# Kernel tuning notes

Hardware: AMD Instinct MI355X
Metric: run time of the kernel (lower is better)

Reference implementation:

```python
import jax, jax.numpy as jnp
import numpy as np

D_IN = 1024
D_OUT = 1024
SEQ = 4096


def setup_inputs() -> dict:
    key = jax.random.key(0)
    kx, kq, kk, kv = jax.random.split(key, 4)
    s = 1.0 / np.sqrt(D_IN)
    return {
        "x": jax.random.normal(kx, (SEQ, D_IN), dtype=jnp.float32),
        # nn.Linear weights: shape [d_out, d_in], applied as x @ W.T
        "W_q": jax.random.uniform(kq, (D_OUT, D_IN), dtype=jnp.float32, minval=-s, maxval=s),
        "W_k": jax.random.uniform(kk, (D_OUT, D_IN), dtype=jnp.float32, minval=-s, maxval=s),
        "W_v": jax.random.uniform(kv, (D_OUT, D_IN), dtype=jnp.float32, minval=-s, maxval=s),
    }


def reference(x, W_q, W_k, W_v):
    # QKV projections (no bias)
    q = x @ W_q.T  # [N, d_out]
    k = x @ W_k.T
    v = x @ W_v.T
    d_k = k.shape[-1]
    scores = (q @ k.T) / jnp.sqrt(jnp.asarray(d_k, x.dtype))  # [N, N]
    attn = jax.nn.softmax(scores, axis=1)
    n = attn.shape[0]
    mask = jnp.tril(jnp.ones((n, n), dtype=attn.dtype))
    causal = attn * mask
    causal = causal / jnp.sum(causal, axis=1, keepdims=True)
    return causal @ v  # [N, d_out]
```

## Files before the change

kernel.cpp:

```cpp
#include <hip/hip_runtime.h>
#include <hip/hip_bf16.h>
#include <stdint.h>
#include <math.h>

#define SEQ 4096
#define DIM 1024

typedef __attribute__((ext_vector_type(8))) __bf16 bf16x8;
typedef __attribute__((ext_vector_type(4))) float f32x4;
typedef __attribute__((ext_vector_type(8))) unsigned short u16x8;

__device__ __forceinline__ unsigned short f2bf(float f) {
  unsigned int u = __float_as_uint(f);
  u = (u + 0x7FFFu + ((u >> 16) & 1u)) >> 16;
  return (unsigned short)u;
}

__device__ __forceinline__ int swz(int o) { return o ^ (((o >> 7) & 7) << 4); }

template <int N> __device__ __forceinline__ void wait_vm() {
  if constexpr (N == 0) asm volatile("s_waitcnt vmcnt(0)" ::: "memory");
  else if constexpr (N == 2) asm volatile("s_waitcnt vmcnt(2)" ::: "memory");
  else if constexpr (N == 4) asm volatile("s_waitcnt vmcnt(4)" ::: "memory");
  else if constexpr (N == 6) asm volatile("s_waitcnt vmcnt(6)" ::: "memory");
  else if constexpr (N == 8) asm volatile("s_waitcnt vmcnt(8)" ::: "memory");
}

__global__ void __launch_bounds__(256) cvt_all(const float* __restrict__ x,
                                               const float* __restrict__ wq,
                                               const float* __restrict__ wk,
                                               const float* __restrict__ wv,
                                               unsigned short* __restrict__ xb,
                                               unsigned short* __restrict__ wqk,
                                               unsigned short* __restrict__ wvb) {
  const int bid = blockIdx.x;
  const float* src;
  unsigned short* dst;
  size_t base;
  if (bid < 2048)      { src = x;  dst = xb;                base = (size_t)bid * 2048; }
  else if (bid < 2560) { src = wq; dst = wqk;               base = (size_t)(bid - 2048) * 2048; }
  else if (bid < 3072) { src = wk; dst = wqk + 1024 * 1024; base = (size_t)(bid - 2560) * 2048; }
  else                 { src = wv; dst = wvb;               base = (size_t)(bid - 3072) * 2048; }
  size_t i = base + (size_t)threadIdx.x * 8;
  float4 a = *reinterpret_cast<const float4*>(src + i);
  float4 b = *reinterpret_cast<const float4*>(src + i + 4);
  u16x8 o;
  o[0] = f2bf(a.x); o[1] = f2bf(a.y); o[2] = f2bf(a.z); o[3] = f2bf(a.w);
  o[4] = f2bf(b.x); o[5] = f2bf(b.y); o[6] = f2bf(b.z); o[7] = f2bf(b.w);
  *reinterpret_cast<u16x8*>(dst + i) = o;
}

__global__ void __launch_bounds__(256) proj_qk(const unsigned short* __restrict__ A,
                                               const unsigned short* __restrict__ B,
                                               unsigned short* __restrict__ C) {
  constexpr int lda = DIM, ldb = DIM, ldc = 2048;
  const int tr = blockIdx.x >> 4, tc = blockIdx.x & 15;

  __shared__ __align__(16) unsigned short As[2][128 * 64];
  __shared__ __align__(16) unsigned short Bs[2][128 * 64];

  const int tid = threadIdx.x;
  const int lane = tid & 63;
  const int wid = tid >> 6;
  const int wr = wid >> 1, wc = wid & 1;
  const int l15 = lane & 15;
  const int kq = lane >> 4;

  f32x4 acc[4][4];
  #pragma unroll
  for (int m = 0; m < 4; ++m)
    #pragma unroll
    for (int n = 0; n < 4; ++n)
      acc[m][n] = (f32x4){0.f, 0.f, 0.f, 0.f};

  const unsigned short* Abase = A + (size_t)tr * 128 * lda;
  const unsigned short* Bbase = B + (size_t)tc * 128 * ldb;

  auto stage = [&](int buf, int kt) {
    const int k0 = kt << 6;
    #pragma unroll
    for (int i = 0; i < 4; ++i) {
      const int o = (i * 256 + tid) * 16;
      const int cs = (swz(o) >> 4) & 7;
      const unsigned short* ga = Abase + (size_t)(o >> 7) * lda + k0 + cs * 8;
      const unsigned short* gb = Bbase + (size_t)(o >> 7) * ldb + k0 + cs * 8;
      __builtin_amdgcn_global_load_lds(
          (const __attribute__((address_space(1))) unsigned int*)ga,
          (__attribute__((address_space(3))) unsigned int*)((char*)&As[buf][0] + o), 16, 0, 0);
      __builtin_amdgcn_global_load_lds(
          (const __attribute__((address_space(1))) unsigned int*)gb,
          (__attribute__((address_space(3))) unsigned int*)((char*)&Bs[buf][0] + o), 16, 0, 0);
    }
  };

  stage(0, 0);
  int cur = 0;
  for (int kt = 0; kt < 16; ++kt) {
    if (kt + 1 < 16) { stage(cur ^ 1, kt + 1); wait_vm<8>(); }
    else wait_vm<0>();
    __builtin_amdgcn_s_barrier();

    bf16x8 af[4][2], bv[4][2];
    #pragma unroll
    for (int m = 0; m < 4; ++m)
      #pragma unroll
      for (int ks = 0; ks < 2; ++ks) {
        const int row = wr * 64 + m * 16 + l15;
        af[m][ks] = *reinterpret_cast<const bf16x8*>(
            (const char*)&As[cur][0] + swz(row * 128 + kq * 16 + ks * 64));
      }
    #pragma unroll
    for (int n = 0; n < 4; ++n)
      #pragma unroll
      for (int ks = 0; ks < 2; ++ks) {
        const int row = wc * 64 + n * 16 + l15;
        bv[n][ks] = *reinterpret_cast<const bf16x8*>(
            (const char*)&Bs[cur][0] + swz(row * 128 + kq * 16 + ks * 64));
      }
    #pragma unroll
    for (int m = 0; m < 4; ++m)
      #pragma unroll
      for (int n = 0; n < 4; ++n) {
        acc[m][n] = __builtin_amdgcn_mfma_f32_16x16x32_bf16(af[m][0], bv[n][0], acc[m][n], 0, 0, 0);
        acc[m][n] = __builtin_amdgcn_mfma_f32_16x16x32_bf16(af[m][1], bv[n][1], acc[m][n], 0, 0, 0);
      }
    __builtin_amdgcn_s_barrier();
    cur ^= 1;
  }

  const int rbase = tr * 128 + wr * 64 + kq * 4;
  const int cbase = tc * 128 + wc * 64 + l15;
  #pragma unroll
  for (int m = 0; m < 4; ++m)
    #pragma unroll
    for (int n = 0; n < 4; ++n)
      #pragma unroll
      for (int i = 0; i < 4; ++i)
        C[(size_t)(rbase + m * 16 + i) * ldc + cbase + n * 16] = f2bf(acc[m][n][i]);
}

__global__ void __launch_bounds__(1024) qkt_vt(const unsigned short* __restrict__ Q,
                                               const unsigned short* __restrict__ K,
                                               unsigned short* __restrict__ S,
                                               const unsigned short* __restrict__ wvb,
                                               const unsigned short* __restrict__ xb,
                                               unsigned short* __restrict__ vt) {
  __shared__ __align__(16) unsigned short As[2][256 * 64];
  __shared__ __align__(16) unsigned short Bs[2][256 * 64];

  const int bid = ((blockIdx.x & 7) << 5) + (blockIdx.x >> 3);
  const int tid = threadIdx.x;
  const int lane = tid & 63;
  const int wid = tid >> 6;
  const int wr = wid >> 2;
  const int wc = wid & 3;
  const int l15 = lane & 15;
  const int kq = lane >> 4;

  if (bid < 136) {
    int tr = (int)((sqrtf(8.0f * bid + 1.0f) - 1.0f) * 0.5f);
    while ((tr + 1) * (tr + 2) / 2 <= bid) ++tr;
    while (tr * (tr + 1) / 2 > bid) --tr;
    const int tc = bid - tr * (tr + 1) / 2;

    constexpr int LDA = 2 * DIM, LDC = SEQ;
    constexpr float SCALE = 0.03125f;

    const unsigned short* Abase = Q + (size_t)tr * 256 * LDA;
    const unsigned short* Bbase = K + (size_t)tc * 256 * LDA;

    f32x4 acc[4][4];
    #pragma unroll
    for (int m = 0; m < 4; ++m)
      #pragma unroll
      for (int n = 0; n < 4; ++n)
        acc[m][n] = (f32x4){0.f, 0.f, 0.f, 0.f};

    auto stage4 = [&](int buf, int kt) {
      const int k0 = kt << 6;
      #pragma unroll
      for (int i = 0; i < 2; ++i) {
        const int ot = (i * 1024 + tid) << 4;
        const int row = ot >> 7;
        const int cs = (swz(ot) >> 4) & 7;
        const unsigned short* ga = Abase + (size_t)row * LDA + k0 + cs * 8;
        const unsigned short* gb = Bbase + (size_t)row * LDA + k0 + cs * 8;
        __builtin_amdgcn_global_load_lds(
            (const __attribute__((address_space(1))) unsigned int*)ga,
            (__attribute__((address_space(3))) unsigned int*)((char*)&As[buf][0] + ot), 16, 0, 0);
        __builtin_amdgcn_global_load_lds(
            (const __attribute__((address_space(1))) unsigned int*)gb,
            (__attribute__((address_space(3))) unsigned int*)((char*)&Bs[buf][0] + ot), 16, 0, 0);
      }
    };

    stage4(0, 0);
    int cur = 0;
    #pragma unroll 1
    for (int kt = 0; kt < 16; ++kt) {
      if (kt + 1 < 16) { stage4(cur ^ 1, kt + 1); wait_vm<4>(); }
      else wait_vm<0>();
      __builtin_amdgcn_s_barrier();

      #pragma unroll
      for (int ks = 0; ks < 2; ++ks) {
        bf16x8 a[4], b[4];
        #pragma unroll
        for (int m = 0; m < 4; ++m) {
          const int row = wr * 64 + m * 16 + l15;
          a[m] = *reinterpret_cast<const bf16x8*>(
              (const char*)&As[cur][0] + swz(row * 128 + kq * 16 + ks * 64));
        }
        #pragma unroll
        for (int n = 0; n < 4; ++n) {
          const int row = wc * 64 + n * 16 + l15;
          b[n] = *reinterpret_cast<const bf16x8*>(
              (const char*)&Bs[cur][0] + swz(row * 128 + kq * 16 + ks * 64));
        }
        __builtin_amdgcn_s_setprio(1);
        #pragma unroll
        for (int m = 0; m < 4; ++m)
          #pragma unroll
          for (int n = 0; n < 4; ++n)
            acc[m][n] = __builtin_amdgcn_mfma_f32_16x16x32_bf16(a[m], b[n], acc[m][n], 0, 0, 0);
        __builtin_amdgcn_s_setprio(0);
      }
      __builtin_amdgcn_s_barrier();
      cur ^= 1;
    }

    const int rb = tr * 256 + wr * 64 + kq * 4;
    const int cb = tc * 256 + wc * 64 + l15;
    #pragma unroll
    for (int m = 0; m < 4; ++m)
      #pragma unroll
      for (int n = 0; n < 4; ++n)
        #pragma unroll
        for (int i = 0; i < 4; ++i)
          S[(size_t)(rb + m * 16 + i) * LDC + cb + n * 16] = f2bf(acc[m][n][i] * SCALE);
    return;
  }

  unsigned short* A0 = &As[0][0];
  unsigned short* B0 = &Bs[0][0];

  for (int t = bid - 136; t < 256; t += 120) {
    const int tr = t >> 5, tc = t & 31;
    const unsigned short* Abase = wvb + (size_t)tr * 128 * DIM;
    const unsigned short* Bbase = xb + (size_t)tc * 128 * DIM;

    f32x4 acc[2][2];
    #pragma unroll
    for (int m = 0; m < 2; ++m)
      #pragma unroll
      for (int n = 0; n < 2; ++n)
        acc[m][n] = (f32x4){0.f, 0.f, 0.f, 0.f};

    auto stage = [&](int buf, int kt) {
      const int k0 = kt << 6;
      const int o = tid << 4;
      const int cs = (swz(o) >> 4) & 7;
      const unsigned short* ga = Abase + (size_t)(o >> 7) * DIM + k0 + cs * 8;
      const unsigned short* gb = Bbase + (size_t)(o >> 7) * DIM + k0 + cs * 8;
      __builtin_amdgcn_global_load_lds(
          (const __attribute__((address_space(1))) unsigned int*)ga,
          (__attribute__((address_space(3))) unsigned int*)((char*)(A0 + buf * 128 * 64) + o), 16, 0, 0);
      __builtin_amdgcn_global_load_lds(
          (const __attribute__((address_space(1))) unsigned int*)gb,
          (__attribute__((address_space(3))) unsigned int*)((char*)(B0 + buf * 128 * 64) + o), 16, 0, 0);
    };

    stage(0, 0);
    int cur = 0;
    for (int kt = 0; kt < 16; ++kt) {
      if (kt + 1 < 16) { stage(cur ^ 1, kt + 1); wait_vm<2>(); }
      else wait_vm<0>();
      __builtin_amdgcn_s_barrier();

      bf16x8 af[2][2], bv[2][2];
      #pragma unroll
      for (int m = 0; m < 2; ++m)
        #pragma unroll
        for (int ks = 0; ks < 2; ++ks) {
          const int row = wr * 32 + m * 16 + l15;
          af[m][ks] = *reinterpret_cast<const bf16x8*>(
              (const char*)(A0 + cur * 128 * 64) + swz(row * 128 + kq * 16 + ks * 64));
        }
      #pragma unroll
      for (int n = 0; n < 2; ++n)
        #pragma unroll
        for (int ks = 0; ks < 2; ++ks) {
          const int row = wc * 32 + n * 16 + l15;
          bv[n][ks] = *reinterpret_cast<const bf16x8*>(
              (const char*)(B0 + cur * 128 * 64) + swz(row * 128 + kq * 16 + ks * 64));
        }
      #pragma unroll
      for (int m = 0; m < 2; ++m)
        #pragma unroll
        for (int n = 0; n < 2; ++n) {
          acc[m][n] = __builtin_amdgcn_mfma_f32_16x16x32_bf16(af[m][0], bv[n][0], acc[m][n], 0, 0, 0);
          acc[m][n] = __builtin_amdgcn_mfma_f32_16x16x32_bf16(af[m][1], bv[n][1], acc[m][n], 0, 0, 0);
        }
      __builtin_amdgcn_s_barrier();
      cur ^= 1;
    }

    const int rbase = tr * 128 + wr * 32 + kq * 4;
    const int cbase = tc * 128 + wc * 32 + l15;
    #pragma unroll
    for (int m = 0; m < 2; ++m)
      #pragma unroll
      for (int n = 0; n < 2; ++n)
        #pragma unroll
        for (int i = 0; i < 4; ++i)
          vt[(size_t)(rbase + m * 16 + i) * SEQ + cbase + n * 16] = f2bf(acc[m][n][i]);
    __builtin_amdgcn_s_barrier();
  }
}

__global__ void __launch_bounds__(256) pv_kernel(const unsigned short* __restrict__ A,
                                                 const unsigned short* __restrict__ B,
                                                 float* __restrict__ C,
                                                 float* __restrict__ P1, float* __restrict__ P2,
                                                 float* __restrict__ P3) {
  constexpr int BM = 64;
  constexpr int lda = SEQ, ldb = SEQ, ldc = DIM;
  int tc = blockIdx.x, tr = blockIdx.y;
  const int s = blockIdx.z;
  const int ltiles = tr + 1;
  int kt0 = s * 16;
  if (kt0 >= ltiles) return;
  const int nt = min(ltiles, kt0 + 16) - kt0;

  __shared__ __align__(16) unsigned short As[2][BM * 64];
  __shared__ __align__(16) unsigned short Bs[2][128 * 64];

  const int tid = threadIdx.x;
  const int lane = tid & 63;
  const int wid = tid >> 6;
  const int wr = wid >> 1, wc = wid & 1;
  const int l15 = lane & 15;
  const int kq = lane >> 4;

  f32x4 acc[2][4];
  #pragma unroll
  for (int m = 0; m < 2; ++m)
    #pragma unroll
    for (int n = 0; n < 4; ++n)
      acc[m][n] = (f32x4){0.f, 0.f, 0.f, 0.f};

  const unsigned short* Abase = A + (size_t)tr * BM * lda;
  const unsigned short* Bbase = B + (size_t)tc * 128 * ldb;

  auto stage = [&](int buf, int ktabs) {
    const int k0 = ktabs << 6;
    #pragma unroll
    for (int i = 0; i < 2; ++i) {
      const int o = (i * 256 + tid) * 16;
      const int cs = (swz(o) >> 4) & 7;
      const unsigned short* g = Abase + (size_t)(o >> 7) * lda + k0 + cs * 8;
      __builtin_amdgcn_global_load_lds(
          (const __attribute__((address_space(1))) unsigned int*)g,
          (__attribute__((address_space(3))) unsigned int*)((char*)&As[buf][0] + o), 16, 0, 0);
    }
    #pragma unroll
    for (int i = 0; i < 4; ++i) {
      const int o = (i * 256 + tid) * 16;
      const int cs = (swz(o) >> 4) & 7;
      const unsigned short* g = Bbase + (size_t)(o >> 7) * ldb + k0 + cs * 8;
      __builtin_amdgcn_global_load_lds(
          (const __attribute__((address_space(1))) unsigned int*)g,
          (__attribute__((address_space(3))) unsigned int*)((char*)&Bs[buf][0] + o), 16, 0, 0);
    }
  };

  stage(0, kt0);
  int cur = 0;
  for (int kt = 0; kt < nt; ++kt) {
    if (kt + 1 < nt) { stage(cur ^ 1, kt0 + kt + 1); wait_vm<6>(); }
    else wait_vm<0>();
    __builtin_amdgcn_s_barrier();

    bf16x8 af[2][2], bv[4][2];
    #pragma unroll
    for (int m = 0; m < 2; ++m)
      #pragma unroll
      for (int ks = 0; ks < 2; ++ks) {
        const int row = wr * 32 + m * 16 + l15;
        af[m][ks] = *reinterpret_cast<const bf16x8*>(
            (const char*)&As[cur][0] + swz(row * 128 + kq * 16 + ks * 64));
      }
    #pragma unroll
    for (int n = 0; n < 4; ++n)
      #pragma unroll
      for (int ks = 0; ks < 2; ++ks) {
        const int row = wc * 64 + n * 16 + l15;
        bv[n][ks] = *reinterpret_cast<const bf16x8*>(
            (const char*)&Bs[cur][0] + swz(row * 128 + kq * 16 + ks * 64));
      }
    #pragma unroll
    for (int m = 0; m < 2; ++m)
      #pragma unroll
      for (int n = 0; n < 4; ++n) {
        acc[m][n] = __builtin_amdgcn_mfma_f32_16x16x32_bf16(af[m][0], bv[n][0], acc[m][n], 0, 0, 0);
        acc[m][n] = __builtin_amdgcn_mfma_f32_16x16x32_bf16(af[m][1], bv[n][1], acc[m][n], 0, 0, 0);
      }
    __builtin_amdgcn_s_barrier();
    cur ^= 1;
  }

  float* fdst = C;
  int rowoff = 0;
  if (s == 1) { fdst = P1; rowoff = 1024; }
  else if (s == 2) { fdst = P2; rowoff = 2048; }
  else if (s == 3) { fdst = P3; rowoff = 3072; }
  const int rbase = tr * BM + wr * 32 + kq * 4;
  const int cbase = tc * 128 + wc * 64 + l15;
  #pragma unroll
  for (int m = 0; m < 2; ++m)
    #pragma unroll
    for (int n = 0; n < 4; ++n)
      #pragma unroll
      for (int i = 0; i < 4; ++i)
        fdst[(size_t)(rbase + m * 16 + i - rowoff) * ldc + cbase + n * 16] = acc[m][n][i];
}

__global__ void __launch_bounds__(256) reduce_kernel(float* __restrict__ out,
                                                     const float* __restrict__ p1,
                                                     const float* __restrict__ p2,
                                                     const float* __restrict__ p3) {
  const int b = blockIdx.x;
  const size_t e = ((size_t)b * 1024) + threadIdx.x * 4;
  f32x4 acc = *reinterpret_cast<f32x4*>(out + (size_t)1024 * 1024 + e);
  acc += *reinterpret_cast<const f32x4*>(p1 + e);
  if (b >= 1024) acc += *reinterpret_cast<const f32x4*>(p2 + e - (size_t)1024 * 1024);
  if (b >= 2048) acc += *reinterpret_cast<const f32x4*>(p3 + e - (size_t)2048 * 1024);
  *reinterpret_cast<f32x4*>(out + (size_t)1024 * 1024 + e) = acc;
}

__global__ void __launch_bounds__(512) softmax_causal2(unsigned short* __restrict__ S) {
  const int g = threadIdx.x >> 8;
  const int row = g ? (SEQ - 1 - blockIdx.x) : blockIdx.x;
  const int tid = threadIdx.x & 255;
  const int lane = threadIdx.x & 63;
  const int wid = (threadIdx.x >> 6) & 3;
  const int limit = ((row >> 6) + 1) << 6;
  unsigned short* Srow = S + (size_t)row * SEQ;

  float vals[16];
  bool act[2];
  #pragma unroll
  for (int i = 0; i < 2; ++i) {
    const int j0 = (tid + i * 256) * 8;
    act[i] = j0 < limit;
    if (act[i]) {
      const uint4 w = *reinterpret_cast<const uint4*>(Srow + j0);
      const unsigned int wb[4] = {w.x, w.y, w.z, w.w};
      #pragma unroll
      for (int e = 0; e < 4; ++e) {
        vals[i * 8 + 2 * e]     = __uint_as_float(wb[e] << 16);
        vals[i * 8 + 2 * e + 1] = __uint_as_float(wb[e] & 0xFFFF0000u);
      }
    } else {
      #pragma unroll
      for (int e = 0; e < 8; ++e) vals[i * 8 + e] = -1e30f;
    }
  }

  float m = -1e30f;
  #pragma unroll
  for (int i = 0; i < 2; ++i)
    #pragma unroll
    for (int e = 0; e < 8; ++e) {
      int j = (tid + i * 256) * 8 + e;
      if (j <= row) m = fmaxf(m, vals[i * 8 + e]);
    }
  #pragma unroll
  for (int off = 32; off > 0; off >>= 1) m = fmaxf(m, __shfl_xor(m, off));
  __shared__ float redm[2][4], reds[2][4];
  if (lane == 0) redm[g][wid] = m;
  __syncthreads();
  m = fmaxf(fmaxf(redm[g][0], redm[g][1]), fmaxf(redm[g][2], redm[g][3]));

  float s = 0.f;
  float ev[16];
  #pragma unroll
  for (int i = 0; i < 2; ++i)
    #pragma unroll
    for (int e = 0; e < 8; ++e) {
      int j = (tid + i * 256) * 8 + e;
      float ex = (j <= row) ? __expf(vals[i * 8 + e] - m) : 0.f;
      ev[i * 8 + e] = ex;
      s += ex;
    }
  #pragma unroll
  for (int off = 32; off > 0; off >>= 1) s += __shfl_xor(s, off);
  if (lane == 0) reds[g][wid] = s;
  __syncthreads();
  s = reds[g][0] + reds[g][1] + reds[g][2] + reds[g][3];
  const float inv = 1.f / s;

  #pragma unroll
  for (int i = 0; i < 2; ++i) {
    if (!act[i]) continue;
    u16x8 o;
    #pragma unroll
    for (int e = 0; e < 8; ++e) o[e] = f2bf(ev[i * 8 + e] * inv);
    *reinterpret_cast<u16x8*>(Srow + (tid + i * 256) * 8) = o;
  }
}

extern "C" void kernel_launch(void* const* d_in, const int* in_sizes, int n_in,
                              void* d_out, int out_size, void* d_ws, size_t ws_size,
                              hipStream_t stream) {
  const float* x  = (const float*)d_in[0];
  const float* Wq = (const float*)d_in[1];
  const float* Wk = (const float*)d_in[2];
  const float* Wv = (const float*)d_in[3];
  float* out = (float*)d_out;

  char* ws = (char*)d_ws;
  const size_t MB = 1u << 20;
  unsigned short* xb   = (unsigned short*)(ws + 0 * MB);
  unsigned short* wqk  = (unsigned short*)(ws + 8 * MB);
  unsigned short* wvb  = (unsigned short*)(ws + 12 * MB);
  unsigned short* qkb  = (unsigned short*)(ws + 14 * MB);
  unsigned short* vt   = (unsigned short*)(ws + 30 * MB);
  unsigned short* S    = (unsigned short*)(ws + 38 * MB);
  float* p1 = (float*)(ws + 0 * MB);
  float* p2 = (float*)(ws + 12 * MB);
  float* p3 = (float*)(ws + 20 * MB);

  cvt_all<<<3584, 256, 0, stream>>>(x, Wq, Wk, Wv, xb, wqk, wvb);

  proj_qk<<<512, 256, 0, stream>>>(xb, wqk, qkb);

  qkt_vt<<<256, 1024, 0, stream>>>(qkb, qkb + 1024, S, wvb, xb, vt);

  softmax_causal2<<<SEQ / 2, 512, 0, stream>>>(S);

  pv_kernel<<<dim3(DIM / 128, SEQ / 64, 4), 256, 0, stream>>>(S, vt, out, p1, p2, p3);
  reduce_kernel<<<3072, 256, 0, stream>>>(out, p1, p2, p3);
}
```

Measured before the change: 125.6 us.

## Fuse causal softmax exp into QK^T epilogue and defer normalization to reduce

Removes the separate softmax kernel. The QK^T epilogue now writes exp(score) directly, zeroing entries above the diagonal in diagonal tiles. Each row's sum is accumulated into a workspace buffer with shuffle reductions plus atomicAdd. The final reduce kernel now covers all rows and divides each output row by its row sum, so the extra read and write pass over the score matrix disappears. It drops the max subtraction, so it depends on scores staying in a range where exp does not overflow, and it adds atomics and a memset.

```diff
diff --git a/kernel.cpp b/kernel.cpp
--- a/kernel.cpp
+++ b/kernel.cpp
@@ -144,7 +144,8 @@
                                                unsigned short* __restrict__ S,
                                                const unsigned short* __restrict__ wvb,
                                                const unsigned short* __restrict__ xb,
-                                               unsigned short* __restrict__ vt) {
+                                               unsigned short* __restrict__ vt,
+                                               float* __restrict__ rowsum) {
   __shared__ __align__(16) unsigned short As[2][256 * 64];
   __shared__ __align__(16) unsigned short Bs[2][256 * 64];
 
@@ -231,13 +232,25 @@
 
     const int rb = tr * 256 + wr * 64 + kq * 4;
     const int cb = tc * 256 + wc * 64 + l15;
+    const bool diag = (tc == tr);
     #pragma unroll
     for (int m = 0; m < 4; ++m)
       #pragma unroll
-      for (int n = 0; n < 4; ++n)
-        #pragma unroll
-        for (int i = 0; i < 4; ++i)
-          S[(size_t)(rb + m * 16 + i) * LDC + cb + n * 16] = f2bf(acc[m][n][i] * SCALE);
+      for (int i = 0; i < 4; ++i) {
+        const int row = rb + m * 16 + i;
+        float rsum = 0.f;
+        #pragma unroll
+        for (int n = 0; n < 4; ++n) {
+          const int col = cb + n * 16;
+          float e = __expf(acc[m][n][i] * SCALE);
+          if (diag && col > row) e = 0.f;
+          rsum += e;
+          S[(size_t)row * LDC + col] = f2bf(e);
+        }
+        #pragma unroll
+        for (int off = 1; off < 16; off <<= 1) rsum += __shfl_xor(rsum, off);
+        if (l15 == 0) atomicAdd(&rowsum[row], rsum);
+      }
     return;
   }
 
@@ -428,86 +441,17 @@
 __global__ void __launch_bounds__(256) reduce_kernel(float* __restrict__ out,
                                                      const float* __restrict__ p1,
                                                      const float* __restrict__ p2,
-                                                     const float* __restrict__ p3) {
-  const int b = blockIdx.x;
-  const size_t e = ((size_t)b * 1024) + threadIdx.x * 4;
-  f32x4 acc = *reinterpret_cast<f32x4*>(out + (size_t)1024 * 1024 + e);
-  acc += *reinterpret_cast<const f32x4*>(p1 + e);
-  if (b >= 1024) acc += *reinterpret_cast<const f32x4*>(p2 + e - (size_t)1024 * 1024);
-  if (b >= 2048) acc += *reinterpret_cast<const f32x4*>(p3 + e - (size_t)2048 * 1024);
-  *reinterpret_cast<f32x4*>(out + (size_t)1024 * 1024 + e) = acc;
-}
-
-__global__ void __launch_bounds__(512) softmax_causal2(unsigned short* __restrict__ S) {
-  const int g = threadIdx.x >> 8;
-  const int row = g ? (SEQ - 1 - blockIdx.x) : blockIdx.x;
-  const int tid = threadIdx.x & 255;
-  const int lane = threadIdx.x & 63;
-  const int wid = (threadIdx.x >> 6) & 3;
-  const int limit = ((row >> 6) + 1) << 6;
-  unsigned short* Srow = S + (size_t)row * SEQ;
-
-  float vals[16];
-  bool act[2];
-  #pragma unroll
-  for (int i = 0; i < 2; ++i) {
-    const int j0 = (tid + i * 256) * 8;
-    act[i] = j0 < limit;
-    if (act[i]) {
-      const uint4 w = *reinterpret_cast<const uint4*>(Srow + j0);
-      const unsigned int wb[4] = {w.x, w.y, w.z, w.w};
-      #pragma unroll
-      for (int e = 0; e < 4; ++e) {
-        vals[i * 8 + 2 * e]     = __uint_as_float(wb[e] << 16);
-        vals[i * 8 + 2 * e + 1] = __uint_as_float(wb[e] & 0xFFFF0000u);
-      }
-    } else {
-      #pragma unroll
-      for (int e = 0; e < 8; ++e) vals[i * 8 + e] = -1e30f;
-    }
-  }
-
-  float m = -1e30f;
-  #pragma unroll
-  for (int i = 0; i < 2; ++i)
-    #pragma unroll
-    for (int e = 0; e < 8; ++e) {
-      int j = (tid + i * 256) * 8 + e;
-      if (j <= row) m = fmaxf(m, vals[i * 8 + e]);
-    }
-  #pragma unroll
-  for (int off = 32; off > 0; off >>= 1) m = fmaxf(m, __shfl_xor(m, off));
-  __shared__ float redm[2][4], reds[2][4];
-  if (lane == 0) redm[g][wid] = m;
-  __syncthreads();
-  m = fmaxf(fmaxf(redm[g][0], redm[g][1]), fmaxf(redm[g][2], redm[g][3]));
-
-  float s = 0.f;
-  float ev[16];
-  #pragma unroll
-  for (int i = 0; i < 2; ++i)
-    #pragma unroll
-    for (int e = 0; e < 8; ++e) {
-      int j = (tid + i * 256) * 8 + e;
-      float ex = (j <= row) ? __expf(vals[i * 8 + e] - m) : 0.f;
-      ev[i * 8 + e] = ex;
-      s += ex;
-    }
-  #pragma unroll
-  for (int off = 32; off > 0; off >>= 1) s += __shfl_xor(s, off);
-  if (lane == 0) reds[g][wid] = s;
-  __syncthreads();
-  s = reds[g][0] + reds[g][1] + reds[g][2] + reds[g][3];
-  const float inv = 1.f / s;
-
-  #pragma unroll
-  for (int i = 0; i < 2; ++i) {
-    if (!act[i]) continue;
-    u16x8 o;
-    #pragma unroll
-    for (int e = 0; e < 8; ++e) o[e] = f2bf(ev[i * 8 + e] * inv);
-    *reinterpret_cast<u16x8*>(Srow + (tid + i * 256) * 8) = o;
-  }
+                                                     const float* __restrict__ p3,
+                                                     const float* __restrict__ rowsum) {
+  const int r = blockIdx.x;
+  const size_t e = ((size_t)r * 1024) + threadIdx.x * 4;
+  f32x4 acc = *reinterpret_cast<f32x4*>(out + e);
+  if (r >= 1024) acc += *reinterpret_cast<const f32x4*>(p1 + e - (size_t)1024 * 1024);
+  if (r >= 2048) acc += *reinterpret_cast<const f32x4*>(p2 + e - (size_t)2048 * 1024);
+  if (r >= 3072) acc += *reinterpret_cast<const f32x4*>(p3 + e - (size_t)3072 * 1024);
+  const float inv = 1.f / rowsum[r];
+  acc *= inv;
+  *reinterpret_cast<f32x4*>(out + e) = acc;
 }
 
 extern "C" void kernel_launch(void* const* d_in, const int* in_sizes, int n_in,
@@ -527,18 +471,19 @@
   unsigned short* qkb  = (unsigned short*)(ws + 14 * MB);
   unsigned short* vt   = (unsigned short*)(ws + 30 * MB);
   unsigned short* S    = (unsigned short*)(ws + 38 * MB);
+  float* rowsum = (float*)(ws + 70 * MB);
   float* p1 = (float*)(ws + 0 * MB);
   float* p2 = (float*)(ws + 12 * MB);
   float* p3 = (float*)(ws + 20 * MB);
 
+  hipMemsetAsync(rowsum, 0, SEQ * sizeof(float), stream);
+
   cvt_all<<<3584, 256, 0, stream>>>(x, Wq, Wk, Wv, xb, wqk, wvb);
 
   proj_qk<<<512, 256, 0, stream>>>(xb, wqk, qkb);
 
-  qkt_vt<<<256, 1024, 0, stream>>>(qkb, qkb + 1024, S, wvb, xb, vt);
-
-  softmax_causal2<<<SEQ / 2, 512, 0, stream>>>(S);
+  qkt_vt<<<256, 1024, 0, stream>>>(qkb, qkb + 1024, S, wvb, xb, vt, rowsum);
 
   pv_kernel<<<dim3(DIM / 128, SEQ / 64, 4), 256, 0, stream>>>(S, vt, out, p1, p2, p3);
-  reduce_kernel<<<3072, 256, 0, stream>>>(out, p1, p2, p3);
-}
+  reduce_kernel<<<SEQ, 256, 0, stream>>>(out, p1, p2, p3, rowsum);
+}
```

Measured after the change: 128.1 us. No clear change (+1.9%).
